# Performance work log

Measured on AMD Instinct MI355X. Metric: run time of the kernel, lower is better.

The kernel has to match this reference:

```python
import jax, jax.numpy as jnp
import numpy as np

GRID = 7
NUM_CLASSES = 80
LAMBDA_COORD = 5.0
LAMBDA_NOOBJ = 0.5
EPS_IOU = 1e-06
EPS_SQRT = 1e-06


def setup_inputs() -> dict:
    key = jax.random.key(0)
    k1, k2, k3 = jax.random.split(key, 3)
    B = 4096
    D = 10 + NUM_CLASSES
    pred = jax.random.uniform(k1, (B, GRID, GRID, D), dtype=jnp.float32)
    target = jax.random.uniform(k2, (B, GRID, GRID, D), dtype=jnp.float32)
    # confidence channel of target must be exactly 1.0 for object cells
    obj = (jax.random.uniform(k3, (B, GRID, GRID)) < 0.25).astype(jnp.float32)
    target = target.at[..., 4].set(obj)
    return {"pred": pred, "target": target}


def _iou(b1, b2):
    # b1, b2: [..., 4] boxes as (cx, cy, w, h) in image coords
    x1, y1, w1, h1 = b1[..., 0], b1[..., 1], b1[..., 2], b1[..., 3]
    x2, y2, w2, h2 = b2[..., 0], b2[..., 1], b2[..., 2], b2[..., 3]
    ix_min = jnp.maximum(x1 - w1 / 2, x2 - w2 / 2)
    iy_min = jnp.maximum(y1 - h1 / 2, y2 - h2 / 2)
    ix_max = jnp.minimum(x1 + w1 / 2, x2 + w2 / 2)
    iy_max = jnp.minimum(y1 + h1 / 2, y2 + h2 / 2)
    iw = jnp.clip(ix_max - ix_min, 0.0)
    ih = jnp.clip(iy_max - iy_min, 0.0)
    inter = iw * ih
    union = w1 * h1 + w2 * h2 - inter
    return inter / (union + EPS_IOU)


def _forward(pred, target):
    S = pred.shape[1]
    gy = jnp.arange(S, dtype=pred.dtype).reshape(1, S, 1)
    gx = jnp.arange(S, dtype=pred.dtype).reshape(1, 1, S)

    def to_img(box5):  # [B,S,S,5] cell-relative -> [B,S,S,4] image coords
        cx = (gx + box5[..., 0]) / S
        cy = (gy + box5[..., 1]) / S
        return jnp.stack([cx, cy, box5[..., 2], box5[..., 3]], axis=-1)

    box1 = pred[..., 0:5]
    box2 = pred[..., 5:10]
    tbox = target[..., 0:5]

    iou1 = _iou(to_img(box1), to_img(tbox))
    iou2 = _iou(to_img(box2), to_img(tbox))
    resp1 = iou1 > iou2  # box1 responsible if strictly greater (matches `if iou1 > iou2`)
    best = jnp.where(resp1[..., None], box1, box2)  # [B,S,S,5]

    obj = target[..., 4] == 1.0  # [B,S,S]
    objf = obj.astype(pred.dtype)
    n_obj = jnp.sum(objf)
    n_cells = jnp.asarray(pred.shape[0] * S * S, pred.dtype)

    # coord: mean-of-2 xy MSE + mean-of-2 sqrt(wh) MSE per responsible box
    dxy2 = jnp.sum((best[..., 0:2] - tbox[..., 0:2]) ** 2, axis=-1)
    swh_p = jnp.sqrt(jnp.clip(best[..., 2:4], EPS_SQRT))
    swh_t = jnp.sqrt(jnp.clip(tbox[..., 2:4], EPS_SQRT))
    dwh2 = jnp.sum((swh_p - swh_t) ** 2, axis=-1)
    coord_per = 0.5 * dxy2 + 0.5 * dwh2
    coord_loss = jnp.sum(coord_per * objf) / jnp.maximum(n_obj, 1.0)

    # confidence: obj cells -> (best_conf - 1)^2 (count 1); noobj -> lam*(c1^2 + c2^2) (count 2)
    conf_obj = (best[..., 4] - 1.0) ** 2
    conf_noobj = LAMBDA_NOOBJ * (pred[..., 4] ** 2 + pred[..., 9] ** 2)
    conf_sum = jnp.sum(jnp.where(obj, conf_obj, conf_noobj))
    conf_count = n_obj + 2.0 * (n_cells - n_obj)
    conf_loss = conf_sum / jnp.maximum(conf_count, 1.0)

    # class: mean over classes per obj cell
    class_per = jnp.mean((pred[..., 10:] - target[..., 10:]) ** 2, axis=-1)
    class_loss = jnp.sum(class_per * objf) / jnp.maximum(n_obj, 1.0)

    return LAMBDA_COORD * coord_loss + conf_loss + class_loss


def reference(pred, target):
    return _forward(pred, target)
```

## Files before the change

kernel.cpp:

```cpp
#include <hip/hip_runtime.h>

#define GRID_S 7
#define NUM_CLASSES 80
#define D_DIM 90
#define LAMBDA_COORD 5.0f
#define LAMBDA_NOOBJ 0.5f
#define EPS_IOU 1e-6f
#define EPS_SQRT 1e-6f

#define TILE 64
#define TILE_F (TILE * D_DIM)
#define TILE_F4 (TILE_F / 4)

__device__ __forceinline__ float iou_img(float cx1, float cy1, float w1, float h1,
                                         float cx2, float cy2, float w2, float h2) {
    float ixmin = fmaxf(cx1 - w1 * 0.5f, cx2 - w2 * 0.5f);
    float iymin = fmaxf(cy1 - h1 * 0.5f, cy2 - h2 * 0.5f);
    float ixmax = fminf(cx1 + w1 * 0.5f, cx2 + w2 * 0.5f);
    float iymax = fminf(cy1 + h1 * 0.5f, cy2 + h2 * 0.5f);
    float iw = fmaxf(ixmax - ixmin, 0.0f);
    float ih = fmaxf(iymax - iymin, 0.0f);
    float inter = iw * ih;
    float uni = w1 * h1 + w2 * h2 - inter;
    return inter / (uni + EPS_IOU);
}

__global__ __launch_bounds__(256) void yolo_cell_kernel(
        const float* __restrict__ pred, const float* __restrict__ targ,
        float* __restrict__ ws, int ncells) {
    __shared__ float sp[TILE_F];
    __shared__ float st[TILE_F];

    const int tid = threadIdx.x;
    const int base_cell = blockIdx.x * TILE;
    const int valid = min(TILE, ncells - base_cell);
    const int nf = valid * D_DIM;

    const size_t base_f = (size_t)base_cell * D_DIM;
    const float4* p4 = (const float4*)(pred + base_f);
    const float4* t4 = (const float4*)(targ + base_f);
    float4* sp4 = (float4*)sp;
    float4* st4 = (float4*)st;
    const int nf4 = nf >> 2;
    for (int i = tid; i < nf4; i += 256) {
        sp4[i] = p4[i];
        st4[i] = t4[i];
    }
    for (int i = (nf4 << 2) + tid; i < nf; i += 256) {
        sp[i] = pred[base_f + i];
        st[i] = targ[base_f + i];
    }
    __syncthreads();

    const int cell = tid & 63;
    const int g = tid >> 6;
    float v_obj = 0.0f, v_coord = 0.0f, v_conf = 0.0f, v_cls = 0.0f;

    if (cell < valid) {
        const float* cp = sp + cell * D_DIM;
        const float* ct = st + cell * D_DIM;
        const float2* cp2 = (const float2*)cp;
        const float2* ct2 = (const float2*)ct;

        float objf = (ct[4] == 1.0f) ? 1.0f : 0.0f;

        float cls = 0.0f;
        const int s2 = 5 + 10 * g;
        #pragma unroll
        for (int j = 0; j < 10; ++j) {
            float2 p = cp2[s2 + j];
            float2 t = ct2[s2 + j];
            float dx = p.x - t.x;
            float dy = p.y - t.y;
            cls = fmaf(dx, dx, cls);
            cls = fmaf(dy, dy, cls);
        }
        v_cls = cls * (1.0f / (float)NUM_CLASSES) * objf;

        if (g == 0) {
            const int gcell = base_cell + cell;
            const int gxy = gcell % (GRID_S * GRID_S);
            const float gy = (float)(gxy / GRID_S);
            const float gx = (float)(gxy % GRID_S);

            float b1x = cp[0], b1y = cp[1], b1w = cp[2], b1h = cp[3], b1c = cp[4];
            float b2x = cp[5], b2y = cp[6], b2w = cp[7], b2h = cp[8], b2c = cp[9];
            float tbx = ct[0], tby = ct[1], tbw = ct[2], tbh = ct[3];

            const float invS = 1.0f / (float)GRID_S;
            float c1x = (gx + b1x) * invS, c1y = (gy + b1y) * invS;
            float c2x = (gx + b2x) * invS, c2y = (gy + b2y) * invS;
            float ctx = (gx + tbx) * invS, cty = (gy + tby) * invS;

            float iou1 = iou_img(c1x, c1y, b1w, b1h, ctx, cty, tbw, tbh);
            float iou2 = iou_img(c2x, c2y, b2w, b2h, ctx, cty, tbw, tbh);
            bool resp1 = iou1 > iou2;

            float bx = resp1 ? b1x : b2x;
            float by = resp1 ? b1y : b2y;
            float bw = resp1 ? b1w : b2w;
            float bh = resp1 ? b1h : b2h;
            float bc = resp1 ? b1c : b2c;

            bool obj = (objf == 1.0f);

            float ddx = bx - tbx, ddy = by - tby;
            float dxy2 = ddx * ddx + ddy * ddy;
            float swpw = sqrtf(fmaxf(bw, EPS_SQRT));
            float swph = sqrtf(fmaxf(bh, EPS_SQRT));
            float swtw = sqrtf(fmaxf(tbw, EPS_SQRT));
            float swth = sqrtf(fmaxf(tbh, EPS_SQRT));
            float dw = swpw - swtw, dh = swph - swth;
            float dwh2 = dw * dw + dh * dh;
            float coord = 0.5f * dxy2 + 0.5f * dwh2;

            float dco = bc - 1.0f;
            float conf_obj = dco * dco;
            float conf_noobj = LAMBDA_NOOBJ * (b1c * b1c + b2c * b2c);

            v_obj = objf;
            v_coord = coord * objf;
            v_conf = obj ? conf_obj : conf_noobj;
        }
    }

    #pragma unroll
    for (int off = 32; off > 0; off >>= 1) {
        v_obj   += __shfl_down(v_obj, off, 64);
        v_coord += __shfl_down(v_coord, off, 64);
        v_conf  += __shfl_down(v_conf, off, 64);
        v_cls   += __shfl_down(v_cls, off, 64);
    }

    __shared__ float red[4][4];
    const int lane = tid & 63;
    const int wid = tid >> 6;
    if (lane == 0) {
        red[wid][0] = v_obj;
        red[wid][1] = v_coord;
        red[wid][2] = v_conf;
        red[wid][3] = v_cls;
    }
    __syncthreads();
    if (tid < 4) {
        float s = red[0][tid] + red[1][tid] + red[2][tid] + red[3][tid];
        atomicAdd(ws + tid, s);
    }
}

__global__ void yolo_final_kernel(const float* __restrict__ ws,
                                  float* __restrict__ out, int ncells) {
    float n_obj = ws[0];
    float coord = ws[1];
    float conf = ws[2];
    float cls = ws[3];
    float n_cells = (float)ncells;
    float conf_count = n_obj + 2.0f * (n_cells - n_obj);
    float denom = fmaxf(n_obj, 1.0f);
    out[0] = LAMBDA_COORD * coord / denom + conf / fmaxf(conf_count, 1.0f) + cls / denom;
}

extern "C" void kernel_launch(void* const* d_in, const int* in_sizes, int n_in,
                              void* d_out, int out_size, void* d_ws, size_t ws_size,
                              hipStream_t stream) {
    const float* pred = (const float*)d_in[0];
    const float* targ = (const float*)d_in[1];
    float* ws = (float*)d_ws;
    float* out = (float*)d_out;

    const int ncells = in_sizes[0] / D_DIM;
    const int ntiles = (ncells + TILE - 1) / TILE;

    hipMemsetAsync(ws, 0, 4 * sizeof(float), stream);
    yolo_cell_kernel<<<ntiles, 256, 0, stream>>>(pred, targ, ws, ncells);
    yolo_final_kernel<<<1, 1, 0, stream>>>(ws, out, ncells);
}
```

Measured before the change: 177.8 us.

## Use direct global-to-LDS loads and replace atomics with per-block partials

Tile staging now uses the global_load_lds builtin, so data goes from global memory straight into shared memory without passing through registers. The cross-block reduction no longer uses four contended float atomics plus a memset. Each block writes its partial sums to the workspace, and a 1024-thread final kernel reduces them. The risk is that the global_load_lds builtin must be lowered and synchronised correctly for the 16-byte width on this target; otherwise the LDS data is wrong.

```diff
diff --git a/kernel.cpp b/kernel.cpp
--- a/kernel.cpp
+++ b/kernel.cpp
@@ -11,6 +11,13 @@
 #define TILE 64
 #define TILE_F (TILE * D_DIM)
 #define TILE_F4 (TILE_F / 4)
+
+__device__ __forceinline__ void async_ld16(const float4* g, float4* l) {
+    __builtin_amdgcn_global_load_lds(
+        (const __attribute__((address_space(1))) void*)g,
+        (__attribute__((address_space(3))) void*)l,
+        16, 0, 0);
+}
 
 __device__ __forceinline__ float iou_img(float cx1, float cy1, float w1, float h1,
                                          float cx2, float cy2, float w2, float h2) {
@@ -27,7 +34,7 @@
 
 __global__ __launch_bounds__(256) void yolo_cell_kernel(
         const float* __restrict__ pred, const float* __restrict__ targ,
-        float* __restrict__ ws, int ncells) {
+        float* __restrict__ part, int ncells) {
     __shared__ float sp[TILE_F];
     __shared__ float st[TILE_F];
 
@@ -35,17 +42,15 @@
     const int base_cell = blockIdx.x * TILE;
     const int valid = min(TILE, ncells - base_cell);
     const int nf = valid * D_DIM;
+    const int nf4 = nf >> 2;
 
     const size_t base_f = (size_t)base_cell * D_DIM;
     const float4* p4 = (const float4*)(pred + base_f);
     const float4* t4 = (const float4*)(targ + base_f);
     float4* sp4 = (float4*)sp;
     float4* st4 = (float4*)st;
-    const int nf4 = nf >> 2;
-    for (int i = tid; i < nf4; i += 256) {
-        sp4[i] = p4[i];
-        st4[i] = t4[i];
-    }
+    for (int i = tid; i < nf4; i += 256) async_ld16(p4 + i, sp4 + i);
+    for (int i = tid; i < nf4; i += 256) async_ld16(t4 + i, st4 + i);
     for (int i = (nf4 << 2) + tid; i < nf; i += 256) {
         sp[i] = pred[base_f + i];
         st[i] = targ[base_f + i];
@@ -144,20 +149,45 @@
     __syncthreads();
     if (tid < 4) {
         float s = red[0][tid] + red[1][tid] + red[2][tid] + red[3][tid];
-        atomicAdd(ws + tid, s);
-    }
-}
-
-__global__ void yolo_final_kernel(const float* __restrict__ ws,
-                                  float* __restrict__ out, int ncells) {
-    float n_obj = ws[0];
-    float coord = ws[1];
-    float conf = ws[2];
-    float cls = ws[3];
-    float n_cells = (float)ncells;
-    float conf_count = n_obj + 2.0f * (n_cells - n_obj);
-    float denom = fmaxf(n_obj, 1.0f);
-    out[0] = LAMBDA_COORD * coord / denom + conf / fmaxf(conf_count, 1.0f) + cls / denom;
+        part[(size_t)blockIdx.x * 4 + tid] = s;
+    }
+}
+
+__global__ __launch_bounds__(1024) void yolo_final_kernel(
+        const float* __restrict__ part, float* __restrict__ out,
+        int nblocks, int ncells) {
+    const int tid = threadIdx.x;
+    float a0 = 0.0f, a1 = 0.0f, a2 = 0.0f, a3 = 0.0f;
+    const float4* p4 = (const float4*)part;
+    for (int b = tid; b < nblocks; b += 1024) {
+        float4 v = p4[b];
+        a0 += v.x; a1 += v.y; a2 += v.z; a3 += v.w;
+    }
+    #pragma unroll
+    for (int off = 32; off > 0; off >>= 1) {
+        a0 += __shfl_down(a0, off, 64);
+        a1 += __shfl_down(a1, off, 64);
+        a2 += __shfl_down(a2, off, 64);
+        a3 += __shfl_down(a3, off, 64);
+    }
+    __shared__ float red[16][4];
+    const int wid = tid >> 6;
+    if ((tid & 63) == 0) {
+        red[wid][0] = a0; red[wid][1] = a1; red[wid][2] = a2; red[wid][3] = a3;
+    }
+    __syncthreads();
+    if (tid == 0) {
+        float n_obj = 0.0f, coord = 0.0f, conf = 0.0f, cls = 0.0f;
+        #pragma unroll
+        for (int w = 0; w < 16; ++w) {
+            n_obj += red[w][0]; coord += red[w][1];
+            conf  += red[w][2]; cls   += red[w][3];
+        }
+        float n_cells = (float)ncells;
+        float conf_count = n_obj + 2.0f * (n_cells - n_obj);
+        float denom = fmaxf(n_obj, 1.0f);
+        out[0] = LAMBDA_COORD * coord / denom + conf / fmaxf(conf_count, 1.0f) + cls / denom;
+    }
 }
 
 extern "C" void kernel_launch(void* const* d_in, const int* in_sizes, int n_in,
@@ -165,13 +195,12 @@
                               hipStream_t stream) {
     const float* pred = (const float*)d_in[0];
     const float* targ = (const float*)d_in[1];
-    float* ws = (float*)d_ws;
+    float* part = (float*)d_ws;
     float* out = (float*)d_out;
 
     const int ncells = in_sizes[0] / D_DIM;
     const int ntiles = (ncells + TILE - 1) / TILE;
 
-    hipMemsetAsync(ws, 0, 4 * sizeof(float), stream);
-    yolo_cell_kernel<<<ntiles, 256, 0, stream>>>(pred, targ, ws, ncells);
-    yolo_final_kernel<<<1, 1, 0, stream>>>(ws, out, ncells);
-}
+    yolo_cell_kernel<<<ntiles, 256, 0, stream>>>(pred, targ, part, ncells);
+    yolo_final_kernel<<<1, 1024, 0, stream>>>(part, out, ntiles, ncells);
+}
```

Measured after the change: 158.4 us. 10.9% less time.
